# Kernel optimization log

Measured on AMD Instinct MI355X. Metric: run time of the kernel, lower is better.

## Reference

```python
import jax, jax.numpy as jnp
import numpy as np
from string import ascii_letters as ABC

N = 12
DIM = 2 ** N
_s = 1.0 / np.sqrt(2.0)
# measurement-basis rotations for X, Y, Z
U_BASIS = jnp.asarray(np.stack([
    np.array([[1, 1], [1, -1]]) * _s,
    np.array([[1, -1j], [1, 1j]]) * _s,
    np.eye(2),
]), dtype=jnp.complex64)


def build_H(params_x, params_zz):
    """Dense transverse-field Ising Hamiltonian: sum_i x_i X_i + sum_i zz_i Z_i Z_{i+1}."""
    basis = jnp.arange(DIM)
    bits = (basis[:, None] >> jnp.arange(N)[None, :]) & 1          # (DIM, N)
    signs = (1 - 2 * bits).astype(jnp.float32)                      # Z eigenvalues
    zz_diag = (signs[:, :-1] * signs[:, 1:]) @ params_zz            # (DIM,)
    flips = basis[:, None] ^ (1 << jnp.arange(N))[None, :]          # (DIM, N)
    rows = jnp.repeat(basis, N)
    cols = flips.reshape(-1)
    vals = jnp.tile(params_x, DIM).astype(jnp.complex64)
    H = jnp.zeros((DIM, DIM), jnp.complex64).at[rows, cols].add(vals)
    return H + jnp.diag(zz_diag.astype(jnp.complex64))


def setup_inputs() -> dict:
    key = jax.random.key(0)
    k1, k2, k3, k4, k5 = jax.random.split(key, 5)
    return {
        "initial_state": 0,
        "ts": jax.random.uniform(k1, (8,), dtype=jnp.float32),
        "pauli_obs": jax.random.randint(k2, (32, N), 0, 3),
        "indices": jax.random.randint(k3, (8, 32, 256), 0, DIM),
        "params_x": jax.random.normal(k4, (N,), dtype=jnp.float32),
        "params_zz": jax.random.normal(k5, (N - 1,), dtype=jnp.float32),
    }


def reference(initial_state, ts, pauli_obs, indices, params_x, params_zz):
    H = build_H(params_x, params_zz)
    rots = U_BASIS[pauli_obs]                    # (B, N, 2, 2)
    ops = [rots[:, i] for i in range(N)]
    subs = ','.join([ABC[1:1 + N]] + [f'a{ABC[1 + N + i]}{ABC[1 + i]}' for i in range(N)]) \
        + '->a' + ABC[1 + N:1 + 2 * N]
    B = pauli_obs.shape[0]

    def one_t(args):
        t, idx = args
        U = jax.scipy.linalg.expm((-1j) * t.astype(jnp.complex64) * H)
        fs = U[:, initial_state].reshape([2] * N)          # state tensor
        rot_state = jnp.einsum(subs, fs, *ops)             # (B, 2, ..., 2)
        probs = jnp.abs(rot_state.reshape(B, DIM)) ** 2    # (B, DIM)
        return jnp.take_along_axis(probs, idx, axis=1)     # (B, shots)

    return jax.lax.map(one_t, (ts, indices))               # (T, B, shots)
```

## Files before the change

### kernel.cpp

```cpp
#include <hip/hip_runtime.h>
#include <math.h>

#define QN 12
#define QDIM 4096
#define CHEB_TOL 2e-3f
#define LSZ (QDIM + 2 * (QDIM / 16))

template <int CTRL>
__device__ __forceinline__ float dppf(float x) {
    int v = __builtin_amdgcn_update_dpp(0, __float_as_int(x), CTRL, 0xF, 0xF, false);
    return __int_as_float(v);
}
#define DPP_QX1 0xB1
#define DPP_QX2 0x4E
#define DPP_QX3 0x1B
#define DPP_HM  0x141
#define DPP_R8  0x128
__device__ __forceinline__ float dpp_x1(float x) { return dppf<DPP_QX1>(x); }
__device__ __forceinline__ float dpp_x2(float x) { return dppf<DPP_QX2>(x); }
__device__ __forceinline__ float dpp_x4(float x) { return dppf<DPP_HM>(dppf<DPP_QX3>(x)); }
__device__ __forceinline__ float dpp_x8(float x) { return dppf<DPP_R8>(x); }

#define CHEB_STEP(T1, T2, CURB, NXTB, KVAL, FVAL, ODD)                        \
    {                                                                          \
        const int   k_ = (KVAL);                                               \
        const float f_ = (FVAL);                                               \
        float4 nbv[5][4];                                                      \
        _Pragma("unroll")                                                      \
        for (int j = 7; j < QN; ++j) {                                         \
            const int gx = g0 ^ (1 << j);                                      \
            const int hx = h0 ^ (1 << (j - 4));                                \
            const float4* q4 = (const float4*)((CURB) + gx + 2 * hx);          \
            _Pragma("unroll")                                                  \
            for (int m = 0; m < 4; ++m) nbv[j - 7][m] = q4[m];                 \
        }                                                                      \
        float hr[8], hi[8];                                                    \
        _Pragma("unroll")                                                      \
        for (int e = 0; e < 8; ++e) {                                          \
            hr[e] = dg[e] * T1[e].x + xj[0] * T1[e ^ 1].x                      \
                  + xj[1] * T1[e ^ 2].x + xj[2] * T1[e ^ 4].x;                 \
            hi[e] = dg[e] * T1[e].y + xj[0] * T1[e ^ 1].y                      \
                  + xj[1] * T1[e ^ 2].y + xj[2] * T1[e ^ 4].y;                 \
            hr[e] += xj[3] * dpp_x1(T1[e].x);  hi[e] += xj[3] * dpp_x1(T1[e].y); \
            hr[e] += xj[4] * dpp_x2(T1[e].x);  hi[e] += xj[4] * dpp_x2(T1[e].y); \
            hr[e] += xj[5] * dpp_x4(T1[e].x);  hi[e] += xj[5] * dpp_x4(T1[e].y); \
            hr[e] += xj[6] * dpp_x8(T1[e].x);  hi[e] += xj[6] * dpp_x8(T1[e].y); \
        }                                                                      \
        _Pragma("unroll")                                                      \
        for (int j = 7; j < QN; ++j) {                                         \
            _Pragma("unroll")                                                  \
            for (int m = 0; m < 4; ++m) {                                      \
                hr[2 * m]     += xj[j] * nbv[j - 7][m].x;                      \
                hi[2 * m]     += xj[j] * nbv[j - 7][m].y;                      \
                hr[2 * m + 1] += xj[j] * nbv[j - 7][m].z;                      \
                hi[2 * m + 1] += xj[j] * nbv[j - 7][m].w;                      \
            }                                                                  \
        }                                                                      \
        const float Jk2 = 2.0f * Jc[k_];                                       \
        const float c_  = (k_ & 2) ? Jk2 : -Jk2;                               \
        _Pragma("unroll")                                                      \
        for (int e = 0; e < 8; ++e) {                                          \
            const float tnx = f_ * hr[e] - T2[e].x;                            \
            const float tny = f_ * hi[e] - T2[e].y;                            \
            T2[e].x = tnx; T2[e].y = tny;                                      \
            if (ODD) {                                                         \
                acc[e].x = fmaf(-c_, tny, acc[e].x);                           \
                acc[e].y = fmaf( c_, tnx, acc[e].y);                           \
            } else {                                                           \
                acc[e].x = fmaf(-c_, tnx, acc[e].x);                           \
                acc[e].y = fmaf(-c_, tny, acc[e].y);                           \
            }                                                                  \
        }                                                                      \
        float4* w_ = (float4*)((NXTB) + l0);                                   \
        _Pragma("unroll")                                                      \
        for (int m = 0; m < 4; ++m)                                            \
            w_[m] = make_float4(T2[2 * m].x, T2[2 * m].y,                      \
                                T2[2 * m + 1].x, T2[2 * m + 1].y);             \
        __syncthreads();                                                       \
    }

__global__ __launch_bounds__(512) void evolve_kernel(
    const int* __restrict__ init_state,
    const float* __restrict__ ts,
    const float* __restrict__ params_x,
    const float* __restrict__ params_zz,
    float2* __restrict__ psi_out)
{
    __shared__ __align__(16) float2 bufA[LSZ];
    __shared__ __align__(16) float2 bufB[LSZ];
    __shared__ float  Jc[128];
    __shared__ float  suLDS[160];
    __shared__ int    dsh;

    const int tid = threadIdx.x;
    const int tI  = blockIdx.x;
    const float t = ts[tI];
    const int g0 = tid * 8;
    const int h0 = g0 >> 4;
    const int l0 = g0 + 2 * h0;

    if (tid < 160) suLDS[tid] = 0.f;

    float xj[QN];
    float bound = 0.f;
#pragma unroll
    for (int j = 0; j < QN; ++j) { xj[j] = params_x[j]; bound += fabsf(xj[j]); }
    float zz[QN - 1];
#pragma unroll
    for (int i = 0; i < QN - 1; ++i) { zz[i] = params_zz[i]; bound += fabsf(zz[i]); }

    float dg[8];
#pragma unroll
    for (int e = 0; e < 8; ++e) {
        const int g = g0 + e;
        float dv = 0.f;
#pragma unroll
        for (int i = 0; i < QN - 1; ++i) {
            const int flip = ((g >> i) ^ (g >> (i + 1))) & 1;
            dv += zz[i] * (1.0f - 2.0f * (float)flip);
        }
        dg[e] = dv;
    }

    const float theta = t * bound;
    int dmax = (int)ceilf(theta + 5.0f * cbrtf(theta)) + 6;
    if (dmax < 8) dmax = 8;
    if (dmax > 126) dmax = 126;

    {
        const int M = dmax + 24;
        const double th = (double)fmaxf(theta, 1e-6f);
        const double invth = 1.0 / th;
        double jkp1 = 0.0, jk = 1e-30, mine = 0.0, nrm = 0.0, suf = 0.0, su_own = 0.0;
        for (int k = M; k >= 0; --k) {
            suf += fabs(jk);
            if (k == tid) { mine = jk; su_own = suf; }
            if (k == 0) nrm += jk;
            else if ((k & 1) == 0) nrm += 2.0 * jk;
            const double jkm1 = (2.0 * (double)k * invth) * jk - jkp1;
            jkp1 = jk; jk = jkm1;
            if (fabs(jk) > 1e250) {
                jk *= 1e-250; jkp1 *= 1e-250; mine *= 1e-250;
                nrm *= 1e-250; suf *= 1e-250; su_own *= 1e-250;
            }
        }
        const double anrm = fabs(nrm);
        if (tid <= dmax) Jc[tid] = (float)(mine / nrm);
        if (tid < 160) suLDS[tid] = (float)(su_own / anrm);
    }

    const int is = init_state[0];
    const float inv_s = 1.0f / bound;

    float2 ta[8];
    float2 tb[8];
    float2 acc[8];
#pragma unroll
    for (int e = 0; e < 8; ++e) {
        const float v = (g0 + e == is) ? 1.0f : 0.0f;
        ta[e] = make_float2(v, 0.f);
        tb[e] = make_float2(0.f, 0.f);
    }
    {
        float4* w0 = (float4*)(bufA + l0);
#pragma unroll
        for (int m = 0; m < 4; ++m)
            w0[m] = make_float4(ta[2 * m].x, ta[2 * m].y,
                                ta[2 * m + 1].x, ta[2 * m + 1].y);
    }
    __syncthreads();

    if (tid < 64) {
        const bool p0 = suLDS[tid + 1] < CHEB_TOL;
        const bool p1 = suLDS[tid + 65] < CHEB_TOL;
        const unsigned long long b0 = __ballot(p0);
        const unsigned long long b1 = __ballot(p1);
        if (tid == 0) {
            int dd;
            if (b0) dd = __ffsll(b0) - 1;
            else if (b1) dd = 64 + __ffsll(b1) - 1;
            else dd = dmax;
            if (dd < 2) dd = 2;
            if (dd > dmax) dd = dmax;
            dsh = dd;
        }
    }
    __syncthreads();
    const int d = dsh;

#pragma unroll
    for (int e = 0; e < 8; ++e) acc[e] = make_float2(Jc[0] * ta[e].x, 0.f);

    CHEB_STEP(ta, tb, bufA, bufB, 1, inv_s, true);
    const float f2 = 2.0f * inv_s;
    int k = 2;
    for (; k + 1 <= d; k += 2) {
        CHEB_STEP(tb, ta, bufB, bufA, k,     f2, false);
        CHEB_STEP(ta, tb, bufA, bufB, k + 1, f2, true);
    }
    if (k <= d) {
        CHEB_STEP(tb, ta, bufB, bufA, k, f2, false);
    }

    float4* o = (float4*)(psi_out + tI * QDIM + g0);
#pragma unroll
    for (int m = 0; m < 4; ++m)
        o[m] = make_float4(acc[2 * m].x, acc[2 * m].y,
                           acc[2 * m + 1].x, acc[2 * m + 1].y);
}

__global__ __launch_bounds__(512) void measure_kernel(
    const float2* __restrict__ psi,
    const int* __restrict__ pauli_obs,
    const int* __restrict__ indices,
    float* __restrict__ out)
{
    __shared__ float2 st[QDIM];
    const int blk = blockIdx.x;
    const int tI = blk >> 5;
    const int b  = blk & 31;

    const float4* src = (const float4*)(psi + tI * QDIM);
    float4* dst = (float4*)st;
    for (int i = threadIdx.x; i < QDIM / 2; i += 512) dst[i] = src[i];
    __syncthreads();

    const float s = 0.70710678118654752440f;
    for (int q = 0; q < QN; ++q) {
        const int p = pauli_obs[b * QN + (QN - 1 - q)];
        if (p == 2) continue;
        const int mask = 1 << q;
        for (int it = threadIdx.x; it < QDIM / 2; it += 512) {
            const int gl = ((it & ~(mask - 1)) << 1) | (it & (mask - 1));
            const int gh = gl | mask;
            const float2 a  = st[gl];
            const float2 c2 = st[gh];
            float2 r0, r1;
            if (p == 0) {
                r0 = make_float2(s * (a.x + c2.x), s * (a.y + c2.y));
                r1 = make_float2(s * (a.x - c2.x), s * (a.y - c2.y));
            } else {
                r0 = make_float2(s * (a.x + c2.y), s * (a.y - c2.x));
                r1 = make_float2(s * (a.x - c2.y), s * (a.y + c2.x));
            }
            st[gl] = r0;
            st[gh] = r1;
        }
        __syncthreads();
    }

    if (threadIdx.x < 256) {
        const int oi = (tI * 32 + b) * 256 + threadIdx.x;
        const int idx = indices[oi];
        const float2 v = st[idx];
        out[oi] = v.x * v.x + v.y * v.y;
    }
}

extern "C" void kernel_launch(void* const* d_in, const int* in_sizes, int n_in,
                              void* d_out, int out_size, void* d_ws, size_t ws_size,
                              hipStream_t stream) {
    const int*   init_state = (const int*)d_in[0];
    const float* ts         = (const float*)d_in[1];
    const int*   pauli_obs  = (const int*)d_in[2];
    const int*   indices    = (const int*)d_in[3];
    const float* params_x   = (const float*)d_in[4];
    const float* params_zz  = (const float*)d_in[5];
    float*  out = (float*)d_out;
    float2* psi = (float2*)d_ws;

    hipLaunchKernelGGL(evolve_kernel, dim3(8), dim3(512), 0, stream,
                       init_state, ts, params_x, params_zz, psi);
    hipLaunchKernelGGL(measure_kernel, dim3(8 * 32), dim3(512), 0, stream,
                       psi, pauli_obs, indices, out);
}
```

Before: 117.0 us.

## Use 1024 threads with 4 amplitudes each in Chebyshev evolve kernel

Doubles the evolve kernel's threads per block from 512 to 1024, so each thread now holds 4 amplitudes instead of 8. The in-register and DPP qubit mapping is remapped: qubits 0-1 in registers, 2-5 via DPP, 6-11 via LDS. It also skips the final LDS write and barrier on the last Chebyshev step. The goal is shorter per-thread serial work and more wavefronts in the latency-bound 8-block kernel, at the cost of more LDS loads per amplitude and heavier barriers across 16 waves.

```diff
diff --git a/kernel.cpp b/kernel.cpp
--- a/kernel.cpp
+++ b/kernel.cpp
@@ -21,45 +21,45 @@
 __device__ __forceinline__ float dpp_x4(float x) { return dppf<DPP_HM>(dppf<DPP_QX3>(x)); }
 __device__ __forceinline__ float dpp_x8(float x) { return dppf<DPP_R8>(x); }
 
-#define CHEB_STEP(T1, T2, CURB, NXTB, KVAL, FVAL, ODD)                        \
+#define CHEB_STEP(T1, T2, CURB, NXTB, KVAL, FVAL, ODD, WRITEB)                \
     {                                                                          \
         const int   k_ = (KVAL);                                               \
         const float f_ = (FVAL);                                               \
-        float4 nbv[5][4];                                                      \
-        _Pragma("unroll")                                                      \
-        for (int j = 7; j < QN; ++j) {                                         \
+        float4 nbv[6][2];                                                      \
+        _Pragma("unroll")                                                      \
+        for (int j = 6; j < QN; ++j) {                                         \
             const int gx = g0 ^ (1 << j);                                      \
             const int hx = h0 ^ (1 << (j - 4));                                \
             const float4* q4 = (const float4*)((CURB) + gx + 2 * hx);          \
+            nbv[j - 6][0] = q4[0];                                             \
+            nbv[j - 6][1] = q4[1];                                             \
+        }                                                                      \
+        float hr[4], hi[4];                                                    \
+        _Pragma("unroll")                                                      \
+        for (int e = 0; e < 4; ++e) {                                          \
+            hr[e] = dg[e] * T1[e].x + xj[0] * T1[e ^ 1].x                      \
+                  + xj[1] * T1[e ^ 2].x;                                       \
+            hi[e] = dg[e] * T1[e].y + xj[0] * T1[e ^ 1].y                      \
+                  + xj[1] * T1[e ^ 2].y;                                       \
+            hr[e] += xj[2] * dpp_x1(T1[e].x);  hi[e] += xj[2] * dpp_x1(T1[e].y); \
+            hr[e] += xj[3] * dpp_x2(T1[e].x);  hi[e] += xj[3] * dpp_x2(T1[e].y); \
+            hr[e] += xj[4] * dpp_x4(T1[e].x);  hi[e] += xj[4] * dpp_x4(T1[e].y); \
+            hr[e] += xj[5] * dpp_x8(T1[e].x);  hi[e] += xj[5] * dpp_x8(T1[e].y); \
+        }                                                                      \
+        _Pragma("unroll")                                                      \
+        for (int j = 6; j < QN; ++j) {                                         \
             _Pragma("unroll")                                                  \
-            for (int m = 0; m < 4; ++m) nbv[j - 7][m] = q4[m];                 \
-        }                                                                      \
-        float hr[8], hi[8];                                                    \
-        _Pragma("unroll")                                                      \
-        for (int e = 0; e < 8; ++e) {                                          \
-            hr[e] = dg[e] * T1[e].x + xj[0] * T1[e ^ 1].x                      \
-                  + xj[1] * T1[e ^ 2].x + xj[2] * T1[e ^ 4].x;                 \
-            hi[e] = dg[e] * T1[e].y + xj[0] * T1[e ^ 1].y                      \
-                  + xj[1] * T1[e ^ 2].y + xj[2] * T1[e ^ 4].y;                 \
-            hr[e] += xj[3] * dpp_x1(T1[e].x);  hi[e] += xj[3] * dpp_x1(T1[e].y); \
-            hr[e] += xj[4] * dpp_x2(T1[e].x);  hi[e] += xj[4] * dpp_x2(T1[e].y); \
-            hr[e] += xj[5] * dpp_x4(T1[e].x);  hi[e] += xj[5] * dpp_x4(T1[e].y); \
-            hr[e] += xj[6] * dpp_x8(T1[e].x);  hi[e] += xj[6] * dpp_x8(T1[e].y); \
-        }                                                                      \
-        _Pragma("unroll")                                                      \
-        for (int j = 7; j < QN; ++j) {                                         \
-            _Pragma("unroll")                                                  \
-            for (int m = 0; m < 4; ++m) {                                      \
-                hr[2 * m]     += xj[j] * nbv[j - 7][m].x;                      \
-                hi[2 * m]     += xj[j] * nbv[j - 7][m].y;                      \
-                hr[2 * m + 1] += xj[j] * nbv[j - 7][m].z;                      \
-                hi[2 * m + 1] += xj[j] * nbv[j - 7][m].w;                      \
+            for (int m = 0; m < 2; ++m) {                                      \
+                hr[2 * m]     += xj[j] * nbv[j - 6][m].x;                      \
+                hi[2 * m]     += xj[j] * nbv[j - 6][m].y;                      \
+                hr[2 * m + 1] += xj[j] * nbv[j - 6][m].z;                      \
+                hi[2 * m + 1] += xj[j] * nbv[j - 6][m].w;                      \
             }                                                                  \
         }                                                                      \
         const float Jk2 = 2.0f * Jc[k_];                                       \
         const float c_  = (k_ & 2) ? Jk2 : -Jk2;                               \
         _Pragma("unroll")                                                      \
-        for (int e = 0; e < 8; ++e) {                                          \
+        for (int e = 0; e < 4; ++e) {                                          \
             const float tnx = f_ * hr[e] - T2[e].x;                            \
             const float tny = f_ * hi[e] - T2[e].y;                            \
             T2[e].x = tnx; T2[e].y = tny;                                      \
@@ -71,15 +71,15 @@
                 acc[e].y = fmaf(-c_, tny, acc[e].y);                           \
             }                                                                  \
         }                                                                      \
-        float4* w_ = (float4*)((NXTB) + l0);                                   \
-        _Pragma("unroll")                                                      \
-        for (int m = 0; m < 4; ++m)                                            \
-            w_[m] = make_float4(T2[2 * m].x, T2[2 * m].y,                      \
-                                T2[2 * m + 1].x, T2[2 * m + 1].y);             \
-        __syncthreads();                                                       \
-    }
-
-__global__ __launch_bounds__(512) void evolve_kernel(
+        if (WRITEB) {                                                          \
+            float4* w_ = (float4*)((NXTB) + l0);                               \
+            w_[0] = make_float4(T2[0].x, T2[0].y, T2[1].x, T2[1].y);           \
+            w_[1] = make_float4(T2[2].x, T2[2].y, T2[3].x, T2[3].y);           \
+            __syncthreads();                                                   \
+        }                                                                      \
+    }
+
+__global__ __launch_bounds__(1024) void evolve_kernel(
     const int* __restrict__ init_state,
     const float* __restrict__ ts,
     const float* __restrict__ params_x,
@@ -95,7 +95,7 @@
     const int tid = threadIdx.x;
     const int tI  = blockIdx.x;
     const float t = ts[tI];
-    const int g0 = tid * 8;
+    const int g0 = tid * 4;
     const int h0 = g0 >> 4;
     const int l0 = g0 + 2 * h0;
 
@@ -109,9 +109,9 @@
 #pragma unroll
     for (int i = 0; i < QN - 1; ++i) { zz[i] = params_zz[i]; bound += fabsf(zz[i]); }
 
-    float dg[8];
-#pragma unroll
-    for (int e = 0; e < 8; ++e) {
+    float dg[4];
+#pragma unroll
+    for (int e = 0; e < 4; ++e) {
         const int g = g0 + e;
         float dv = 0.f;
 #pragma unroll
@@ -152,21 +152,19 @@
     const int is = init_state[0];
     const float inv_s = 1.0f / bound;
 
-    float2 ta[8];
-    float2 tb[8];
-    float2 acc[8];
-#pragma unroll
-    for (int e = 0; e < 8; ++e) {
+    float2 ta[4];
+    float2 tb[4];
+    float2 acc[4];
+#pragma unroll
+    for (int e = 0; e < 4; ++e) {
         const float v = (g0 + e == is) ? 1.0f : 0.0f;
         ta[e] = make_float2(v, 0.f);
         tb[e] = make_float2(0.f, 0.f);
     }
     {
         float4* w0 = (float4*)(bufA + l0);
-#pragma unroll
-        for (int m = 0; m < 4; ++m)
-            w0[m] = make_float4(ta[2 * m].x, ta[2 * m].y,
-                                ta[2 * m + 1].x, ta[2 * m + 1].y);
+        w0[0] = make_float4(ta[0].x, ta[0].y, ta[1].x, ta[1].y);
+        w0[1] = make_float4(ta[2].x, ta[2].y, ta[3].x, ta[3].y);
     }
     __syncthreads();
 
@@ -189,24 +187,22 @@
     const int d = dsh;
 
 #pragma unroll
-    for (int e = 0; e < 8; ++e) acc[e] = make_float2(Jc[0] * ta[e].x, 0.f);
-
-    CHEB_STEP(ta, tb, bufA, bufB, 1, inv_s, true);
+    for (int e = 0; e < 4; ++e) acc[e] = make_float2(Jc[0] * ta[e].x, 0.f);
+
+    CHEB_STEP(ta, tb, bufA, bufB, 1, inv_s, true, (1 < d));
     const float f2 = 2.0f * inv_s;
     int k = 2;
     for (; k + 1 <= d; k += 2) {
-        CHEB_STEP(tb, ta, bufB, bufA, k,     f2, false);
-        CHEB_STEP(ta, tb, bufA, bufB, k + 1, f2, true);
+        CHEB_STEP(tb, ta, bufB, bufA, k,     f2, false, true);
+        CHEB_STEP(ta, tb, bufA, bufB, k + 1, f2, true,  (k + 1 < d));
     }
     if (k <= d) {
-        CHEB_STEP(tb, ta, bufB, bufA, k, f2, false);
+        CHEB_STEP(tb, ta, bufB, bufA, k, f2, false, false);
     }
 
     float4* o = (float4*)(psi_out + tI * QDIM + g0);
-#pragma unroll
-    for (int m = 0; m < 4; ++m)
-        o[m] = make_float4(acc[2 * m].x, acc[2 * m].y,
-                           acc[2 * m + 1].x, acc[2 * m + 1].y);
+    o[0] = make_float4(acc[0].x, acc[0].y, acc[1].x, acc[1].y);
+    o[1] = make_float4(acc[2].x, acc[2].y, acc[3].x, acc[3].y);
 }
 
 __global__ __launch_bounds__(512) void measure_kernel(
@@ -269,7 +265,7 @@
     float*  out = (float*)d_out;
     float2* psi = (float2*)d_ws;
 
-    hipLaunchKernelGGL(evolve_kernel, dim3(8), dim3(512), 0, stream,
+    hipLaunchKernelGGL(evolve_kernel, dim3(8), dim3(1024), 0, stream,
                        init_state, ts, params_x, params_zz, psi);
     hipLaunchKernelGGL(measure_kernel, dim3(8 * 32), dim3(512), 0, stream,
                        psi, pauli_obs, indices, out);
```

After: 116.3 us. No clear change (-0.6%).
